# Performance work log

Measured on AMD Instinct MI355X. Metric: run time of the kernel, lower is better.

The kernel has to match this reference:

```python
import jax, jax.numpy as jnp
import numpy as np

TEMPERATURE = 8.0  # sqrt(d_k) with d_k=64
NEG = -9e15        # matches torch zero_vec constant -9000000000000000.0


def setup_inputs() -> dict:
    key = jax.random.key(0)
    k1, k2, k3, k4 = jax.random.split(key, 4)
    a, b, N, d = 32, 4, 1024, 64  # a = nhead*b, nhead = 8
    q = jax.random.normal(k1, (a, N, d), dtype=jnp.float32)
    k = jax.random.normal(k2, (a, N, d), dtype=jnp.float32)
    v = jax.random.normal(k3, (a, N, d), dtype=jnp.float32)
    adj = jax.random.randint(k4, (b, N, N), 0, 2, dtype=jnp.int32)
    return {"q": q, "k": k, "v": v, "adj": adj}


def reference(q, k, v, adj):
    # q,k,v: [nhead*b, N, d]; adj: [b, N, N]
    a, N, d = v.shape
    b = adj.shape[0]
    nhead = a // b
    # scores: [a, N, N]
    attn = jnp.einsum('bnd,bmd->bnm', q, k) / jnp.asarray(TEMPERATURE, q.dtype)
    # 'local' focus: mask by adjacency, broadcast over heads (head-major layout
    # matches torch's adj.unsqueeze(0).repeat(nhead,1,1,1).view(-1,N,N))
    attn = attn.reshape(nhead, b, N, N)
    attn = jnp.where(adj[None] > 0, attn, jnp.asarray(NEG, attn.dtype))
    attn = attn.reshape(a, N, N)
    attn = jax.nn.softmax(attn, axis=2)
    # dropout p=0.0 -> identity
    output = jnp.einsum('bnm,bmd->bnd', attn, v)
    return (output, attn)
```

## Files before the change

### kernel.cpp

```cpp
#include <hip/hip_runtime.h>
#include <hip/hip_bf16.h>

#define A_TOT 32
#define SEQ 1024
#define DIM 64
#define NT 16
#define GSTRIDE 1056
#define TILEB (8 * GSTRIDE)

typedef __attribute__((ext_vector_type(8))) short short8;
typedef __attribute__((ext_vector_type(4))) float f32x4;
typedef unsigned long long u64;

static __device__ __forceinline__ unsigned pack2bf(float a, float b) {
    union { __hip_bfloat16 h[2]; unsigned u; } x;
    x.h[0] = __float2bfloat16(a);
    x.h[1] = __float2bfloat16(b);
    return x.u;
}

static __device__ __forceinline__ void gload_lds16(const void* g, void* l) {
    __builtin_amdgcn_global_load_lds(
        (const __attribute__((address_space(1))) unsigned*)g,
        (__attribute__((address_space(3))) unsigned*)l, 16, 0, 0);
}

static __device__ __forceinline__ short8 lds_frag(const unsigned char* tile,
                                                  int row, int chunk) {
    const int byte = (row >> 3) * GSTRIDE + (row & 7) * 128 +
                     ((chunk ^ (row & 7)) << 4);
    return *reinterpret_cast<const short8*>(tile + byte);
}

#define WAITBAR(N) do {                                          \
    asm volatile("s_waitcnt vmcnt(" #N ")" ::: "memory");        \
    __builtin_amdgcn_sched_barrier(0);                           \
    __builtin_amdgcn_s_barrier();                                \
    __builtin_amdgcn_sched_barrier(0);                           \
    asm volatile("" ::: "memory");                               \
} while (0)

__global__ void prepass_kernel(const float* __restrict__ q,
                               const float* __restrict__ k,
                               const float* __restrict__ v,
                               const int* __restrict__ adj,
                               __hip_bfloat16* __restrict__ qb,
                               __hip_bfloat16* __restrict__ kb,
                               __hip_bfloat16* __restrict__ vt,
                               u64* __restrict__ adjm) {
    __shared__ __hip_bfloat16 tile[64][65];
    const int tid = threadIdx.x;
    if (blockIdx.y < 2) {
        const float* src = blockIdx.y ? k : q;
        __hip_bfloat16* dst = blockIdx.y ? kb : qb;
        int i = (blockIdx.x * 256 + tid) * 4;
        float4 f = *reinterpret_cast<const float4*>(src + i);
        union { __hip_bfloat16 h[4]; ushort4 u; } cv;
        cv.h[0] = __float2bfloat16(f.x);
        cv.h[1] = __float2bfloat16(f.y);
        cv.h[2] = __float2bfloat16(f.z);
        cv.h[3] = __float2bfloat16(f.w);
        *reinterpret_cast<ushort4*>(dst + i) = cv.u;
        return;
    }
    if (blockIdx.x < 512) {
        const int bh = blockIdx.x >> 4;
        const int n0 = (blockIdx.x & 15) * 64;
        const float* vsrc = v + ((size_t)bh * SEQ + n0) * DIM;
        for (int e = tid; e < 64 * 64; e += 256) {
            int i = e >> 6;
            int d = e & 63;
            tile[i][d] = __float2bfloat16(vsrc[(size_t)i * DIM + d]);
        }
        __syncthreads();
        __hip_bfloat16* vdst = vt + (size_t)bh * DIM * SEQ + n0;
        for (int e = tid; e < 64 * 64; e += 256) {
            int d = e >> 6;
            int i = e & 63;
            vdst[(size_t)d * SEQ + i] = tile[i][d];
        }
        return;
    }
    if (blockIdx.x < 1536) {
        const int px   = blockIdx.x - 512;
        const int wv   = tid >> 6;
        const int lane = tid & 63;
        const int wbase = px * 64 + wv * 16;
        for (int it = 0; it < 16; ++it) {
            const int w = wbase + it;
            const int a = adj[(size_t)w * 64 + lane];
            u64 m = __ballot(a > 0);
            if (lane == 0) adjm[w] = m;
        }
    }
}

__launch_bounds__(256)
__global__ void lsum_kernel(const __hip_bfloat16* __restrict__ qb,
                            const __hip_bfloat16* __restrict__ kb,
                            const u64* __restrict__ adjm,
                            float* __restrict__ lpart) {
    __shared__ __align__(16) unsigned char kstage[2][TILEB];
    __shared__ float part[4][4][16];

    const int wg    = (blockIdx.x & 7) * 256 + (blockIdx.x >> 3);
    const int bh    = wg >> 6;
    const int lidx  = wg & 63;
    const int rb    = lidx >> 2;
    const int kq    = lidx & 3;
    const int batch = bh & 3;
    const int tid   = threadIdx.x;
    const int wid   = tid >> 6;
    const int lane  = tid & 63;
    const int lr    = lane & 15;
    const int lgi   = lane >> 4;
    const int row16 = rb * 64 + wid * 16;
    const int t0    = kq * 4;

    const int sub  = lane >> 3;
    const int csrc = (lane & 7) ^ sub;

    const __hip_bfloat16* qrow = qb + ((size_t)bh * SEQ + row16 + lr) * DIM + lgi * 8;
    const short8 qf0 = *reinterpret_cast<const short8*>(qrow);
    const short8 qf1 = *reinterpret_cast<const short8*>(qrow + 32);

    const u64* mrow = adjm + ((size_t)batch * SEQ + row16 + lr) * (SEQ / 64);
    const __hip_bfloat16* kbh = kb + (size_t)bh * SEQ * DIM;
    const int kperm = (lr >> 2) * 8 + (lr & 3);

    auto stageK = [&](int t, int b) {
        const __hip_bfloat16* g0 = kbh + (size_t)(t * 64 + wid * 16) * DIM;
        unsigned char* l0 = &kstage[b][(wid * 2) * GSTRIDE];
        gload_lds16(g0 + (size_t)sub * DIM + csrc * 8, l0);
        gload_lds16(g0 + (size_t)(8 + sub) * DIM + csrc * 8, l0 + GSTRIDE);
    };

    u64 mb = mrow[t0], mn_ = 0;
    stageK(t0, 0);
    WAITBAR(0);

    float lp = 0.f;
    int cur = 0;
#pragma unroll
    for (int i = 0; i < 4; ++i) {
        const int t = t0 + i;
        if (i < 3) {
            mn_ = mrow[t + 1];
            stageK(t + 1, cur ^ 1);
        }
#pragma unroll
        for (int c = 0; c < 4; ++c) {
            const int cb = (c >> 1) * 32 + (c & 1) * 4;
            const int krow = cb + kperm;
            short8 kf0 = lds_frag(kstage[cur], krow, lgi);
            short8 kf1 = lds_frag(kstage[cur], krow, 4 + lgi);
            f32x4 acc = {0.f, 0.f, 0.f, 0.f};
            acc = __builtin_amdgcn_mfma_f32_16x16x32_bf16(kf0, qf0, acc, 0, 0, 0);
            acc = __builtin_amdgcn_mfma_f32_16x16x32_bf16(kf1, qf1, acc, 0, 0, 0);
            const unsigned b4 = (unsigned)(mb >> (cb + lgi * 8)) & 0xFu;
            float p0 = (b4 & 1u) ? __expf(acc[0] * 0.125f) : 0.f;
            float p1 = (b4 & 2u) ? __expf(acc[1] * 0.125f) : 0.f;
            float p2 = (b4 & 4u) ? __expf(acc[2] * 0.125f) : 0.f;
            float p3 = (b4 & 8u) ? __expf(acc[3] * 0.125f) : 0.f;
            lp += (p0 + p1) + (p2 + p3);
        }
        if (i < 3) {
            mb = mn_;
            WAITBAR(0);
        }
        cur ^= 1;
    }

    part[wid][lgi][lr] = lp;
    asm volatile("" ::: "memory");
    if (lane < 16) {
        float s = part[wid][0][lane] + part[wid][1][lane] +
                  part[wid][2][lane] + part[wid][3][lane];
        lpart[((size_t)kq * A_TOT + bh) * SEQ + row16 + lane] = s;
    }
}

__launch_bounds__(256)
__global__ void graph_attn_kernel(const __hip_bfloat16* __restrict__ qb,
                                  const __hip_bfloat16* __restrict__ kb,
                                  const __hip_bfloat16* __restrict__ vt,
                                  const u64* __restrict__ adjm,
                                  const float* __restrict__ lpart,
                                  float* __restrict__ out,
                                  float* __restrict__ attn) {
    __shared__ __align__(16) unsigned char kstage[2][TILEB];
    __shared__ __align__(16) unsigned char vstage[2][TILEB];

    const int wg    = (blockIdx.x & 7) * 64 + (blockIdx.x >> 3);
    const int bh    = wg >> 4;
    const int rb    = wg & 15;
    const int batch = bh & 3;
    const int tid   = threadIdx.x;
    const int wid   = tid >> 6;
    const int lane  = tid & 63;
    const int lr    = lane & 15;
    const int lgi   = lane >> 4;
    const int row16 = rb * 64 + wid * 16;

    const int sub  = lane >> 3;
    const int csrc = (lane & 7) ^ sub;

    const __hip_bfloat16* qrow = qb + ((size_t)bh * SEQ + row16 + lr) * DIM + lgi * 8;
    const short8 qf0 = *reinterpret_cast<const short8*>(qrow);
    const short8 qf1 = *reinterpret_cast<const short8*>(qrow + 32);

    const u64* mrow = adjm + ((size_t)batch * SEQ + row16 + lr) * (SEQ / 64);
    const __hip_bfloat16* kbh = kb + (size_t)bh * SEQ * DIM;
    const __hip_bfloat16* vth = vt + (size_t)bh * DIM * SEQ;

    const int kperm = (lr >> 2) * 8 + (lr & 3);

    auto stageK = [&](int t, int b) {
        const __hip_bfloat16* g0 = kbh + (size_t)(t * 64 + wid * 16) * DIM;
        unsigned char* l0 = &kstage[b][(wid * 2) * GSTRIDE];
        gload_lds16(g0 + (size_t)sub * DIM + csrc * 8, l0);
        gload_lds16(g0 + (size_t)(8 + sub) * DIM + csrc * 8, l0 + GSTRIDE);
    };
    auto stageV = [&](int t, int b) {
        const __hip_bfloat16* g0 = vth + (size_t)(wid * 16) * SEQ + t * 64;
        unsigned char* l0 = &vstage[b][(wid * 2) * GSTRIDE];
        gload_lds16(g0 + (size_t)sub * SEQ + csrc * 8, l0);
        gload_lds16(g0 + (size_t)(8 + sub) * SEQ + csrc * 8, l0 + GSTRIDE);
    };

    const float* lpr = lpart + (size_t)bh * SEQ + row16 + lr;
    const float a0 = lpr[0];
    const float a1 = lpr[(size_t)A_TOT * SEQ];
    const float a2 = lpr[(size_t)2 * A_TOT * SEQ];
    const float a3 = lpr[(size_t)3 * A_TOT * SEQ];

    u64 mb = mrow[0], mn_ = 0;
    stageK(0, 0); stageV(0, 0);
    WAITBAR(0);

    const float linv = 1.0f / (((a0 + a1) + (a2 + a3)) + 1e-37f);

    f32x4 o[4];
#pragma unroll
    for (int c = 0; c < 4; ++c) o[c] = (f32x4){0.f, 0.f, 0.f, 0.f};

    float* attn_row = attn + (size_t)bh * SEQ * SEQ + (size_t)(row16 + lr) * SEQ;
    unsigned pk[4][2];
    int cur = 0;
    for (int t = 0; t < NT; ++t) {
        if (t < NT - 1) {
            mn_ = mrow[t + 1];
            stageK(t + 1, cur ^ 1);
            stageV(t + 1, cur ^ 1);
        }
        __builtin_amdgcn_sched_barrier(0);
#pragma unroll
        for (int c = 0; c < 4; ++c) {
            const int cb = (c >> 1) * 32 + (c & 1) * 4;
            const int krow = cb + kperm;
            short8 kf0 = lds_frag(kstage[cur], krow, lgi);
            short8 kf1 = lds_frag(kstage[cur], krow, 4 + lgi);
            f32x4 acc = {0.f, 0.f, 0.f, 0.f};
            acc = __builtin_amdgcn_mfma_f32_16x16x32_bf16(kf0, qf0, acc, 0, 0, 0);
            acc = __builtin_amdgcn_mfma_f32_16x16x32_bf16(kf1, qf1, acc, 0, 0, 0);
            const unsigned b4 = (unsigned)(mb >> (cb + lgi * 8)) & 0xFu;
            float p0 = (b4 & 1u) ? __expf(acc[0] * 0.125f) * linv : 0.f;
            float p1 = (b4 & 2u) ? __expf(acc[1] * 0.125f) * linv : 0.f;
            float p2 = (b4 & 4u) ? __expf(acc[2] * 0.125f) * linv : 0.f;
            float p3 = (b4 & 8u) ? __expf(acc[3] * 0.125f) * linv : 0.f;
            *reinterpret_cast<float4*>(attn_row + t * 64 + cb + lgi * 8) =
                (float4){p0, p1, p2, p3};
            pk[c][0] = pack2bf(p0, p1);
            pk[c][1] = pack2bf(p2, p3);
        }
        union { unsigned u[4]; short8 s; } pf0, pf1;
        pf0.u[0] = pk[0][0]; pf0.u[1] = pk[0][1];
        pf0.u[2] = pk[1][0]; pf0.u[3] = pk[1][1];
        pf1.u[0] = pk[2][0]; pf1.u[1] = pk[2][1];
        pf1.u[2] = pk[3][0]; pf1.u[3] = pk[3][1];
#pragma unroll
        for (int c2 = 0; c2 < 4; ++c2) {
            const int vrow = c2 * 16 + lr;
            short8 vf0 = lds_frag(vstage[cur], vrow, lgi);
            short8 vf1 = lds_frag(vstage[cur], vrow, 4 + lgi);
            o[c2] = __builtin_amdgcn_mfma_f32_16x16x32_bf16(pf0.s, vf0, o[c2], 0, 0, 0);
            o[c2] = __builtin_amdgcn_mfma_f32_16x16x32_bf16(pf1.s, vf1, o[c2], 0, 0, 0);
        }
        if (t < NT - 1) {
            mb = mn_;
            WAITBAR(4);
        }
        cur ^= 1;
    }

    float* ob = out + (size_t)bh * SEQ * DIM + (size_t)row16 * DIM;
#pragma unroll
    for (int c2 = 0; c2 < 4; ++c2)
#pragma unroll
        for (int j = 0; j < 4; ++j)
            ob[(size_t)(lgi * 4 + j) * DIM + c2 * 16 + lr] = o[c2][j];
}

extern "C" void kernel_launch(void* const* d_in, const int* in_sizes, int n_in,
                              void* d_out, int out_size, void* d_ws, size_t ws_size,
                              hipStream_t stream) {
    const float* q   = (const float*)d_in[0];
    const float* k   = (const float*)d_in[1];
    const float* v   = (const float*)d_in[2];
    const int*   adj = (const int*)d_in[3];

    float* out  = (float*)d_out;
    float* attn = out + (size_t)A_TOT * SEQ * DIM;

    __hip_bfloat16* qb = (__hip_bfloat16*)d_ws;
    __hip_bfloat16* kb = qb + (size_t)A_TOT * SEQ * DIM;
    __hip_bfloat16* vt = kb + (size_t)A_TOT * SEQ * DIM;
    u64* adjm = (u64*)(vt + (size_t)A_TOT * SEQ * DIM);
    float* lpart = (float*)(adjm + 4 * SEQ * (SEQ / 64));

    prepass_kernel<<<dim3(2048, 3), 256, 0, stream>>>(q, k, v, adj, qb, kb, vt, adjm);
    lsum_kernel<<<2048, 256, 0, stream>>>(qb, kb, adjm, lpart);
    graph_attn_kernel<<<512, 256, 0, stream>>>(qb, kb, vt, adjm, lpart, out, attn);
}
```

Before: 62.61 us.

## Process K/V tiles in pairs with four-slot LDS ring to halve barriers

Expands the K/V LDS staging from two to four buffers and restructures the main loop to compute two 64-column tiles per iteration while prefetching the next two. This halves the number of wait/barrier points and deepens the prefetch, aiming to hide global load latency. It doubles LDS use per workgroup, which may reduce occupancy.

```diff
diff --git a/kernel.cpp b/kernel.cpp
--- a/kernel.cpp
+++ b/kernel.cpp
@@ -188,8 +188,8 @@
                                   const float* __restrict__ lpart,
                                   float* __restrict__ out,
                                   float* __restrict__ attn) {
-    __shared__ __align__(16) unsigned char kstage[2][TILEB];
-    __shared__ __align__(16) unsigned char vstage[2][TILEB];
+    __shared__ __align__(16) unsigned char kstage[4][TILEB];
+    __shared__ __align__(16) unsigned char vstage[4][TILEB];
 
     const int wg    = (blockIdx.x & 7) * 64 + (blockIdx.x >> 3);
     const int bh    = wg >> 4;
@@ -234,8 +234,9 @@
     const float a2 = lpr[(size_t)2 * A_TOT * SEQ];
     const float a3 = lpr[(size_t)3 * A_TOT * SEQ];
 
-    u64 mb = mrow[0], mn_ = 0;
+    u64 mb0 = mrow[0], mb1 = mrow[1];
     stageK(0, 0); stageV(0, 0);
+    stageK(1, 1); stageV(1, 1);
     WAITBAR(0);
 
     const float linv = 1.0f / (((a0 + a1) + (a2 + a3)) + 1e-37f);
@@ -245,25 +246,19 @@
     for (int c = 0; c < 4; ++c) o[c] = (f32x4){0.f, 0.f, 0.f, 0.f};
 
     float* attn_row = attn + (size_t)bh * SEQ * SEQ + (size_t)(row16 + lr) * SEQ;
-    unsigned pk[4][2];
-    int cur = 0;
-    for (int t = 0; t < NT; ++t) {
-        if (t < NT - 1) {
-            mn_ = mrow[t + 1];
-            stageK(t + 1, cur ^ 1);
-            stageV(t + 1, cur ^ 1);
-        }
-        __builtin_amdgcn_sched_barrier(0);
+
+    auto compute_tile = [&](int t, int slot, u64 m) {
+        unsigned pk[4][2];
 #pragma unroll
         for (int c = 0; c < 4; ++c) {
             const int cb = (c >> 1) * 32 + (c & 1) * 4;
             const int krow = cb + kperm;
-            short8 kf0 = lds_frag(kstage[cur], krow, lgi);
-            short8 kf1 = lds_frag(kstage[cur], krow, 4 + lgi);
+            short8 kf0 = lds_frag(kstage[slot], krow, lgi);
+            short8 kf1 = lds_frag(kstage[slot], krow, 4 + lgi);
             f32x4 acc = {0.f, 0.f, 0.f, 0.f};
             acc = __builtin_amdgcn_mfma_f32_16x16x32_bf16(kf0, qf0, acc, 0, 0, 0);
             acc = __builtin_amdgcn_mfma_f32_16x16x32_bf16(kf1, qf1, acc, 0, 0, 0);
-            const unsigned b4 = (unsigned)(mb >> (cb + lgi * 8)) & 0xFu;
+            const unsigned b4 = (unsigned)(m >> (cb + lgi * 8)) & 0xFu;
             float p0 = (b4 & 1u) ? __expf(acc[0] * 0.125f) * linv : 0.f;
             float p1 = (b4 & 2u) ? __expf(acc[1] * 0.125f) * linv : 0.f;
             float p2 = (b4 & 4u) ? __expf(acc[2] * 0.125f) * linv : 0.f;
@@ -281,16 +276,30 @@
 #pragma unroll
         for (int c2 = 0; c2 < 4; ++c2) {
             const int vrow = c2 * 16 + lr;
-            short8 vf0 = lds_frag(vstage[cur], vrow, lgi);
-            short8 vf1 = lds_frag(vstage[cur], vrow, 4 + lgi);
+            short8 vf0 = lds_frag(vstage[slot], vrow, lgi);
+            short8 vf1 = lds_frag(vstage[slot], vrow, 4 + lgi);
             o[c2] = __builtin_amdgcn_mfma_f32_16x16x32_bf16(pf0.s, vf0, o[c2], 0, 0, 0);
             o[c2] = __builtin_amdgcn_mfma_f32_16x16x32_bf16(pf1.s, vf1, o[c2], 0, 0, 0);
         }
-        if (t < NT - 1) {
-            mb = mn_;
-            WAITBAR(4);
-        }
-        cur ^= 1;
+    };
+
+    for (int p = 0; p < NT / 2; ++p) {
+        const int s0 = (p & 1) * 2;
+        u64 mn0 = 0, mn1 = 0;
+        if (p < NT / 2 - 1) {
+            mn0 = mrow[2 * p + 2];
+            mn1 = mrow[2 * p + 3];
+            const int d0 = s0 ^ 2;
+            stageK(2 * p + 2, d0);     stageV(2 * p + 2, d0);
+            stageK(2 * p + 3, d0 + 1); stageV(2 * p + 3, d0 + 1);
+        }
+        __builtin_amdgcn_sched_barrier(0);
+        compute_tile(2 * p,     s0,     mb0);
+        compute_tile(2 * p + 1, s0 + 1, mb1);
+        if (p < NT / 2 - 1) {
+            mb0 = mn0; mb1 = mn1;
+            WAITBAR(8);
+        }
     }
 
     float* ob = out + (size_t)bh * SEQ * DIM + (size_t)row16 * DIM;
```

Measured after the change: 62.08 us. No clear change (-0.9%).
